# Kernel optimization log

Measured on AMD Instinct MI355X. Metric: run time of the kernel, lower is better.

## Reference

```python
import jax, jax.numpy as jnp
import numpy as np

N_SENS, N_HID, N_MOT = 10000, 400000, 1000
E_SH, E_HH, E_HM = 4_000_000, 16_000_000, 400_000
BETA, THR, SLOPE = 0.9, 1.0, 25.0  # snn.Leaky(beta, threshold), surrogate.fast_sigmoid(slope=25)

# Heaviside spike with fast-sigmoid surrogate gradient (matches snnTorch)
@jax.custom_vjp
def spike(x):
    return (x > 0).astype(x.dtype)

def _spike_fwd(x):
    return (x > 0).astype(x.dtype), x

def _spike_bwd(x, g):
    return (g / (SLOPE * jnp.abs(x) + 1.0) ** 2,)

spike.defvjp(_spike_fwd, _spike_bwd)

def lif(inp, mem):
    # snn.Leaky, reset_mechanism='zero': mem = beta*mem + I; spike; reset to 0 where spiked
    mem = BETA * mem + inp
    spk = spike(mem - THR)
    mem = mem - jax.lax.stop_gradient(spk) * mem  # reset detached, as in snnTorch
    return spk, mem

def spmm_t(pre_idx, post_idx, w, pre_spikes, n_post):
    # torch.sparse.mm(W^T, pre_spikes): gather pre activity along edges, scatter-add to post
    contrib = w * pre_spikes[pre_idx]          # [E]
    return jax.ops.segment_sum(contrib, post_idx, num_segments=n_post)

def setup_inputs() -> dict:
    key = jax.random.key(0)
    ks = jax.random.split(key, 16)
    std_sh = 1.0 / np.sqrt(N_SENS * 0.001)
    std_hh = 1.0 / np.sqrt(N_HID * 0.0001)
    std_hm = 1.0 / np.sqrt(N_HID * 0.001)
    return {
        "sensory_input": jax.random.uniform(ks[0], (N_SENS,), jnp.float32),
        "sensory_mem": jax.random.uniform(ks[1], (N_SENS,), jnp.float32),
        "hidden_mem": jax.random.uniform(ks[2], (N_HID,), jnp.float32),
        "motor_mem": jax.random.uniform(ks[3], (N_MOT,), jnp.float32),
        "hidden_prev_spikes": (jax.random.uniform(ks[4], (N_HID,)) < 0.05).astype(jnp.float32),
        "w_sh": jax.random.normal(ks[5], (E_SH,), jnp.float32) * std_sh,
        "w_hh": jax.random.normal(ks[6], (E_HH,), jnp.float32) * std_hh,
        "w_hm": jax.random.normal(ks[7], (E_HM,), jnp.float32) * std_hm,
        "sh_pre": jax.random.randint(ks[8], (E_SH,), 0, N_SENS, jnp.int32),
        "sh_post": jax.random.randint(ks[9], (E_SH,), 0, N_HID, jnp.int32),
        "hh_pre": jax.random.randint(ks[10], (E_HH,), 0, N_HID, jnp.int32),
        "hh_post": jax.random.randint(ks[11], (E_HH,), 0, N_HID, jnp.int32),
        "hm_pre": jax.random.randint(ks[12], (E_HM,), 0, N_HID, jnp.int32),
        "hm_post": jax.random.randint(ks[13], (E_HM,), 0, N_MOT, jnp.int32),
    }

def reference(sensory_input, sensory_mem, hidden_mem, motor_mem, hidden_prev_spikes,
              w_sh, w_hh, w_hm, sh_pre, sh_post, hh_pre, hh_post, hm_pre, hm_post):
    sens_spk, _ = lif(sensory_input * 5.0, sensory_mem)
    hid_in = spmm_t(sh_pre, sh_post, w_sh, sens_spk, N_HID)
    hid_in = hid_in + 0.5 * spmm_t(hh_pre, hh_post, w_hh, hidden_prev_spikes, N_HID)
    hid_spk, _ = lif(hid_in * 5.0, hidden_mem)
    mot_in = spmm_t(hm_pre, hm_post, w_hm, hid_spk, N_MOT)
    mot_spk, _ = lif(mot_in * 20.0, motor_mem)
    return mot_spk
```

## Files before the change

kernel.cpp:

```cpp
#include <hip/hip_runtime.h>


#define N_SENS 10000
#define N_HID  400000
#define N_MOT  1000

#define CHUNK_LOG 14
#define CHUNK     (1 << CHUNK_LOG)
#define NBUCKET   25
#define CAP       196608
#define NCOPY     20

#define SENS_MW   320
#define HID_MW    12512

#define BUF_SH    4096
#define BUF_HH    2048
#define EPT_SH    4
#define EPT_HH    8

#define NB_HM     128

__global__ void make_masks(const float* __restrict__ sens_in,
                           const float* __restrict__ sens_mem,
                           const float* __restrict__ hid_prev,
                           uint2* __restrict__ smask,
                           uint2* __restrict__ hmask,
                           float* __restrict__ extra,
                           int* __restrict__ cursors, int nb_sens) {
    bool pred = false;
    int i;
    uint2* dst;
    int maxw;
    if ((int)blockIdx.x < nb_sens) {
        if (blockIdx.x == 0 && threadIdx.x < 32) cursors[threadIdx.x] = 0;
        i = blockIdx.x * blockDim.x + threadIdx.x;
        if (i < N_SENS) pred = (0.9f * sens_mem[i] + 5.0f * sens_in[i]) > 1.0f;
        dst = smask; maxw = SENS_MW / 2;
    } else {
        i = (blockIdx.x - nb_sens) * blockDim.x + threadIdx.x;
        if (i < N_HID) { pred = (hid_prev[i] != 0.0f); extra[i] = 0.0f; }
        dst = hmask; maxw = HID_MW / 2;
    }
    unsigned long long b = __ballot(pred);
    if ((threadIdx.x & 63) == 0) {
        int w = i >> 6;
        if (w < maxw) dst[w] = make_uint2((unsigned)b, (unsigned)(b >> 32));
    }
}

template <int MW, int BUFCAP, int EPT>
__global__ __launch_bounds__(1024, 8)
void bin_gather(const int* __restrict__ pre, const int* __restrict__ post,
                const float* __restrict__ w, const unsigned* __restrict__ gmask,
                int n_e, float scale,
                uint2* __restrict__ pairs, int* __restrict__ gcursor,
                float* __restrict__ extra) {
    __shared__ unsigned sm[MW];
    __shared__ uint2 buf[BUFCAP];
    __shared__ int h[4][32];
    __shared__ int gb[32];
    __shared__ int lcur[32];
    __shared__ int total;

    const int tid = threadIdx.x;
    const int lane = tid & 63;
    for (int i = tid; i < MW / 4; i += 1024)
        ((uint4*)sm)[i] = ((const uint4*)gmask)[i];
    if (tid < 128) ((int*)h)[tid] = 0;
    if (tid == 0) total = 0;
    __syncthreads();

    const int base = blockIdx.x * (1024 * EPT) + tid;

    int pr[EPT];
    #pragma unroll
    for (int j = 0; j < EPT; ++j) {
        int e = base + j * 1024;
        pr[j] = (e < n_e) ? pre[e] : -1;
    }
    bool act[EPT];
    #pragma unroll
    for (int j = 0; j < EPT; ++j)
        act[j] = (pr[j] >= 0) && ((sm[pr[j] >> 5] >> (pr[j] & 31)) & 1u);
    unsigned p[EPT]; float wv[EPT];
    #pragma unroll
    for (int j = 0; j < EPT; ++j) {
        p[j] = 0; wv[j] = 0.0f;
        if (act[j]) {
            int e = base + j * 1024;
            p[j] = (unsigned)post[e];
            wv[j] = scale * w[e];
        }
    }
    #pragma unroll
    for (int j = 0; j < EPT; ++j) {
        unsigned long long m = __ballot(act[j]);
        if (!m) continue;
        int rank = __popcll(m & ((1ull << lane) - 1ull));
        int bse = 0;
        if (lane == 0) bse = atomicAdd(&total, __popcll(m));
        bse = __shfl(bse, 0);
        if (act[j]) {
            int k = bse + rank;
            if (k < BUFCAP) buf[k] = make_uint2(p[j], __float_as_uint(wv[j]));
            else atomicAdd(&extra[p[j]], wv[j]);
        }
    }
    __syncthreads();
    int tot = total; if (tot > BUFCAP) tot = BUFCAP;

    int rep = (tid >> 6) & 3;
    for (int k = tid; k < tot; k += 1024)
        atomicAdd(&h[rep][buf[k].x >> CHUNK_LOG], 1);
    __syncthreads();
    if (tid < NBUCKET) {
        int hb = h[0][tid] + h[1][tid] + h[2][tid] + h[3][tid];
        gb[tid] = hb ? atomicAdd(&gcursor[tid], hb) : 0;
        lcur[tid] = 0;
    }
    __syncthreads();

    for (int k = tid; k < tot; k += 1024) {
        uint2 u = buf[k];
        int b = u.x >> CHUNK_LOG;
        int s = atomicAdd(&lcur[b], 1);
        int pos = gb[b] + s;
        if (pos < CAP)
            pairs[(size_t)b * CAP + pos] =
                make_uint2(u.x & (CHUNK - 1), u.y);
        else
            atomicAdd(&extra[u.x], __uint_as_float(u.y));
    }
}

__global__ __launch_bounds__(1024, 8)
void accum_bucket(const uint2* __restrict__ pairs,
                  const int* __restrict__ cursors,
                  float* __restrict__ partials) {
    int bucket = blockIdx.x / NCOPY;
    int copy   = blockIdx.x % NCOPY;
    __shared__ float acc[CHUNK];
    for (int i = threadIdx.x; i < CHUNK; i += blockDim.x) acc[i] = 0.0f;
    __syncthreads();

    int count = cursors[bucket];
    if (count > CAP) count = CAP;
    int begin = (int)((long long)count * copy / NCOPY);
    int end   = (int)((long long)count * (copy + 1) / NCOPY);
    const uint2* src = pairs + (size_t)bucket * CAP;
    for (int i = begin + threadIdx.x; i < end; i += blockDim.x) {
        uint2 u = src[i];
        atomicAdd(&acc[u.x], __uint_as_float(u.y));
    }
    __syncthreads();
    float* dst = partials + ((size_t)bucket * NCOPY + copy) * CHUNK;
    for (int i = threadIdx.x; i < CHUNK; i += blockDim.x) dst[i] = acc[i];
}

__global__ void reduce_lif_hidden_mask(const float* __restrict__ partials,
                                       const float* __restrict__ extra,
                                       const float* __restrict__ mem,
                                       uint2* __restrict__ mask) {
    int i = blockIdx.x * blockDim.x + threadIdx.x;
    bool pred = false;
    if (i < N_HID) {
        int b = i >> CHUNK_LOG, local = i & (CHUNK - 1);
        const float* p = partials + (size_t)b * NCOPY * CHUNK + local;
        float sum = extra[i];
        #pragma unroll
        for (int c = 0; c < NCOPY; ++c) sum += p[(size_t)c * CHUNK];
        pred = (0.9f * mem[i] + 5.0f * sum) > 1.0f;
    }
    unsigned long long bal = __ballot(pred);
    if ((threadIdx.x & 63) == 0) {
        int w = i >> 6;
        if (w < HID_MW / 2)
            mask[w] = make_uint2((unsigned)bal, (unsigned)(bal >> 32));
    }
}

__global__ __launch_bounds__(512, 8)
void scatter_motor_mask(const int* __restrict__ pre,
                        const int* __restrict__ post,
                        const float* __restrict__ w,
                        const unsigned* __restrict__ gmask,
                        float* __restrict__ partials, int n_edges) {
    __shared__ float acc[N_MOT];
    for (int j = threadIdx.x; j < N_MOT; j += blockDim.x) acc[j] = 0.0f;
    __syncthreads();
    for (int e = blockIdx.x * blockDim.x + threadIdx.x; e < n_edges;
         e += gridDim.x * blockDim.x) {
        int pr = pre[e];
        if ((gmask[pr >> 5] >> (pr & 31)) & 1u)
            atomicAdd(&acc[post[e]], w[e]);
    }
    __syncthreads();
    float* out = partials + (size_t)blockIdx.x * N_MOT;
    for (int j = threadIdx.x; j < N_MOT; j += blockDim.x) out[j] = acc[j];
}

__global__ void reduce_lif_motor(const float* __restrict__ partials, int nb,
                                 const float* __restrict__ mem,
                                 float* __restrict__ out) {
    int m = blockIdx.x * blockDim.x + threadIdx.x;
    if (m >= N_MOT) return;
    float sum = 0.0f;
    for (int b = 0; b < nb; ++b) sum += partials[(size_t)b * N_MOT + m];
    float v = 0.9f * mem[m] + 20.0f * sum;
    out[m] = (v > 1.0f) ? 1.0f : 0.0f;
}

__global__ void lif_kernel(const float* __restrict__ inp,
                           const float* __restrict__ mem_in,
                           float* __restrict__ spk,
                           float scale, int n) {
    int i = blockIdx.x * blockDim.x + threadIdx.x;
    if (i < n) {
        float m = 0.9f * mem_in[i] + scale * inp[i];
        spk[i] = (m > 1.0f) ? 1.0f : 0.0f;
    }
}

__global__ void scatter_dev(const int* __restrict__ pre,
                            const int* __restrict__ post,
                            const float* __restrict__ w,
                            const float* __restrict__ spikes,
                            float* __restrict__ out,
                            float scale, int n_edges) {
    int e = blockIdx.x * blockDim.x + threadIdx.x;
    if (e >= n_edges) return;
    float s = spikes[pre[e]];
    if (s != 0.0f) atomicAdd(&out[post[e]], scale * w[e] * s);
}

__global__ void lif_hidden_direct(const float* __restrict__ hid_in,
                                  const float* __restrict__ mem,
                                  float* __restrict__ spk) {
    int i = blockIdx.x * blockDim.x + threadIdx.x;
    if (i >= N_HID) return;
    float m = 0.9f * mem[i] + 5.0f * hid_in[i];
    spk[i] = (m > 1.0f) ? 1.0f : 0.0f;
}

__global__ void scatter_motor_f(const int* __restrict__ pre,
                                const int* __restrict__ post,
                                const float* __restrict__ w,
                                const float* __restrict__ spikes,
                                float* __restrict__ partials, int n_edges) {
    __shared__ float acc[N_MOT];
    for (int j = threadIdx.x; j < N_MOT; j += blockDim.x) acc[j] = 0.0f;
    __syncthreads();
    for (int e = blockIdx.x * blockDim.x + threadIdx.x; e < n_edges;
         e += gridDim.x * blockDim.x) {
        float s = spikes[pre[e]];
        if (s != 0.0f) atomicAdd(&acc[post[e]], w[e] * s);
    }
    __syncthreads();
    float* out = partials + (size_t)blockIdx.x * N_MOT;
    for (int j = threadIdx.x; j < N_MOT; j += blockDim.x) out[j] = acc[j];
}

extern "C" void kernel_launch(void* const* d_in, const int* in_sizes, int n_in,
                              void* d_out, int out_size, void* d_ws, size_t ws_size,
                              hipStream_t stream) {
    const float* sensory_input = (const float*)d_in[0];
    const float* sensory_mem   = (const float*)d_in[1];
    const float* hidden_mem    = (const float*)d_in[2];
    const float* motor_mem     = (const float*)d_in[3];
    const float* hidden_prev   = (const float*)d_in[4];
    const float* w_sh          = (const float*)d_in[5];
    const float* w_hh          = (const float*)d_in[6];
    const float* w_hm          = (const float*)d_in[7];
    const int*   sh_pre        = (const int*)d_in[8];
    const int*   sh_post       = (const int*)d_in[9];
    const int*   hh_pre        = (const int*)d_in[10];
    const int*   hh_post       = (const int*)d_in[11];
    const int*   hm_pre        = (const int*)d_in[12];
    const int*   hm_post       = (const int*)d_in[13];
    const int e_sh = in_sizes[5];
    const int e_hh = in_sizes[6];
    const int e_hm = in_sizes[7];
    const int B = 256;

    size_t o_cursor = 0;
    size_t o_extra  = 32;
    size_t o_pairs  = o_extra + N_HID;
    size_t o_part   = o_pairs + (size_t)NBUCKET * CAP * 2;
    size_t o_smask  = o_part + (size_t)NBUCKET * NCOPY * CHUNK;
    size_t o_hmaskp = o_smask + SENS_MW;
    size_t o_hmasks = o_hmaskp + HID_MW;
    size_t o_mpart  = o_hmasks + HID_MW;
    size_t f_need   = o_mpart + (size_t)NB_HM * N_MOT;
    bool fast = (ws_size / sizeof(float)) >= f_need;

    float* ws = (float*)d_ws;
    if (fast) {
        int*      cursors = (int*)(ws + o_cursor);
        float*    extra   = ws + o_extra;
        uint2*    pairs   = (uint2*)(ws + o_pairs);
        float*    part    = ws + o_part;
        unsigned* smask   = (unsigned*)(ws + o_smask);
        unsigned* hmaskp  = (unsigned*)(ws + o_hmaskp);
        unsigned* hmasks  = (unsigned*)(ws + o_hmasks);
        float*    mpart   = ws + o_mpart;

        int nb_sens = (N_SENS + B - 1) / B;
        int nb_hidm = (N_HID + B - 1) / B;
        make_masks<<<nb_sens + nb_hidm, B, 0, stream>>>(
            sensory_input, sensory_mem, hidden_prev,
            (uint2*)smask, (uint2*)hmaskp, extra, cursors, nb_sens);

        int nb_sh = (e_sh + 1024 * EPT_SH - 1) / (1024 * EPT_SH);
        int nb_hh = (e_hh + 1024 * EPT_HH - 1) / (1024 * EPT_HH);
        bin_gather<SENS_MW, BUF_SH, EPT_SH><<<nb_sh, 1024, 0, stream>>>(
            sh_pre, sh_post, w_sh, smask, e_sh, 1.0f, pairs, cursors, extra);
        bin_gather<HID_MW, BUF_HH, EPT_HH><<<nb_hh, 1024, 0, stream>>>(
            hh_pre, hh_post, w_hh, hmaskp, e_hh, 0.5f, pairs, cursors, extra);

        accum_bucket<<<NBUCKET * NCOPY, 1024, 0, stream>>>(pairs, cursors, part);
        reduce_lif_hidden_mask<<<(N_HID + B - 1) / B, B, 0, stream>>>(
            part, extra, hidden_mem, (uint2*)hmasks);
        scatter_motor_mask<<<NB_HM, 512, 0, stream>>>(
            hm_pre, hm_post, w_hm, hmasks, mpart, e_hm);
        reduce_lif_motor<<<(N_MOT + B - 1) / B, B, 0, stream>>>(
            mpart, NB_HM, motor_mem, (float*)d_out);
    } else {
        float* hid_in   = ws;
        float* sens_spk = hid_in + N_HID;
        float* hid_spk  = sens_spk + 10016;
        float* mpart    = hid_spk + N_HID;
        hipMemsetAsync(hid_in, 0, (size_t)N_HID * sizeof(float), stream);
        lif_kernel<<<(N_SENS + B - 1) / B, B, 0, stream>>>(
            sensory_input, sensory_mem, sens_spk, 5.0f, N_SENS);
        scatter_dev<<<(e_sh + B - 1) / B, B, 0, stream>>>(
            sh_pre, sh_post, w_sh, sens_spk, hid_in, 1.0f, e_sh);
        scatter_dev<<<(e_hh + B - 1) / B, B, 0, stream>>>(
            hh_pre, hh_post, w_hh, hidden_prev, hid_in, 0.5f, e_hh);
        lif_hidden_direct<<<(N_HID + B - 1) / B, B, 0, stream>>>(
            hid_in, hidden_mem, hid_spk);
        scatter_motor_f<<<NB_HM, B, 0, stream>>>(
            hm_pre, hm_post, w_hm, hid_spk, mpart, e_hm);
        reduce_lif_motor<<<(N_MOT + B - 1) / B, B, 0, stream>>>(
            mpart, NB_HM, motor_mem, (float*)d_out);
    }
}
```

Baseline: 356.4 us.

## Compact active edges per thread with wave scan, retune tiles, cache motor mask in LDS

The binning kernel now builds a per-thread bitmask of active edges and uses one wave-wide prefix scan plus one shared atomic per wave to reserve buffer slots. This replaces a ballot and atomic per unrolled slot and loads post and weight only for active edges. Edges per thread rise (8 for sensory, 32 for recurrent), the sensory buffer doubles, and accumulation copies and motor blocks are halved. The motor scatter now stages the hidden spike mask in shared memory and runs 1024-thread blocks. Fewer, larger blocks may reduce parallelism and latency hiding, and higher per-block counts raise the chance of overflow into global atomics.

```diff
diff --git a/kernel.cpp b/kernel.cpp
--- a/kernel.cpp
+++ b/kernel.cpp
@@ -9,17 +9,17 @@
 #define CHUNK     (1 << CHUNK_LOG)
 #define NBUCKET   25
 #define CAP       196608
-#define NCOPY     20
+#define NCOPY     10
 
 #define SENS_MW   320
 #define HID_MW    12512
 
-#define BUF_SH    4096
+#define EPT_SH    8
+#define BUF_SH    8192
+#define EPT_HH    32
 #define BUF_HH    2048
-#define EPT_SH    4
-#define EPT_HH    8
-
-#define NB_HM     128
+
+#define NB_HM     64
 
 __global__ void make_masks(const float* __restrict__ sens_in,
                            const float* __restrict__ sens_mem,
@@ -51,11 +51,11 @@
 
 template <int MW, int BUFCAP, int EPT>
 __global__ __launch_bounds__(1024, 8)
-void bin_gather(const int* __restrict__ pre, const int* __restrict__ post,
-                const float* __restrict__ w, const unsigned* __restrict__ gmask,
-                int n_e, float scale,
-                uint2* __restrict__ pairs, int* __restrict__ gcursor,
-                float* __restrict__ extra) {
+void bin_scan(const int* __restrict__ pre, const int* __restrict__ post,
+              const float* __restrict__ w, const unsigned* __restrict__ gmask,
+              int n_e, float scale,
+              uint2* __restrict__ pairs, int* __restrict__ gcursor,
+              float* __restrict__ extra) {
     __shared__ unsigned sm[MW];
     __shared__ uint2 buf[BUFCAP];
     __shared__ int h[4][32];
@@ -73,38 +73,38 @@
 
     const int base = blockIdx.x * (1024 * EPT) + tid;
 
-    int pr[EPT];
+    unsigned am = 0;
     #pragma unroll
     for (int j = 0; j < EPT; ++j) {
         int e = base + j * 1024;
-        pr[j] = (e < n_e) ? pre[e] : -1;
-    }
-    bool act[EPT];
+        if (e < n_e) {
+            int pr = pre[e];
+            if ((sm[pr >> 5] >> (pr & 31)) & 1u) am |= (1u << j);
+        }
+    }
+    int cnt = __popc(am);
+
+    int inc = cnt;
     #pragma unroll
-    for (int j = 0; j < EPT; ++j)
-        act[j] = (pr[j] >= 0) && ((sm[pr[j] >> 5] >> (pr[j] & 31)) & 1u);
-    unsigned p[EPT]; float wv[EPT];
+    for (int d = 1; d < 64; d <<= 1) {
+        int n = __shfl_up(inc, d);
+        if (lane >= d) inc += n;
+    }
+    int wtot = __shfl(inc, 63);
+    int wbase = 0;
+    if (lane == 63 && wtot) wbase = atomicAdd(&total, wtot);
+    wbase = __shfl(wbase, 63);
+    int off = wbase + inc - cnt;
+
     #pragma unroll
     for (int j = 0; j < EPT; ++j) {
-        p[j] = 0; wv[j] = 0.0f;
-        if (act[j]) {
+        if ((am >> j) & 1u) {
             int e = base + j * 1024;
-            p[j] = (unsigned)post[e];
-            wv[j] = scale * w[e];
-        }
-    }
-    #pragma unroll
-    for (int j = 0; j < EPT; ++j) {
-        unsigned long long m = __ballot(act[j]);
-        if (!m) continue;
-        int rank = __popcll(m & ((1ull << lane) - 1ull));
-        int bse = 0;
-        if (lane == 0) bse = atomicAdd(&total, __popcll(m));
-        bse = __shfl(bse, 0);
-        if (act[j]) {
-            int k = bse + rank;
-            if (k < BUFCAP) buf[k] = make_uint2(p[j], __float_as_uint(wv[j]));
-            else atomicAdd(&extra[p[j]], wv[j]);
+            unsigned p = (unsigned)post[e];
+            float wv = scale * w[e];
+            if (off < BUFCAP) buf[off] = make_uint2(p, __float_as_uint(wv));
+            else atomicAdd(&extra[p], wv);
+            ++off;
         }
     }
     __syncthreads();
@@ -180,19 +180,22 @@
     }
 }
 
-__global__ __launch_bounds__(512, 8)
+__global__ __launch_bounds__(1024, 8)
 void scatter_motor_mask(const int* __restrict__ pre,
                         const int* __restrict__ post,
                         const float* __restrict__ w,
                         const unsigned* __restrict__ gmask,
                         float* __restrict__ partials, int n_edges) {
     __shared__ float acc[N_MOT];
+    __shared__ unsigned sm[HID_MW];
+    for (int i = threadIdx.x; i < HID_MW / 4; i += blockDim.x)
+        ((uint4*)sm)[i] = ((const uint4*)gmask)[i];
     for (int j = threadIdx.x; j < N_MOT; j += blockDim.x) acc[j] = 0.0f;
     __syncthreads();
     for (int e = blockIdx.x * blockDim.x + threadIdx.x; e < n_edges;
          e += gridDim.x * blockDim.x) {
         int pr = pre[e];
-        if ((gmask[pr >> 5] >> (pr & 31)) & 1u)
+        if ((sm[pr >> 5] >> (pr & 31)) & 1u)
             atomicAdd(&acc[post[e]], w[e]);
     }
     __syncthreads();
@@ -313,15 +316,15 @@
 
         int nb_sh = (e_sh + 1024 * EPT_SH - 1) / (1024 * EPT_SH);
         int nb_hh = (e_hh + 1024 * EPT_HH - 1) / (1024 * EPT_HH);
-        bin_gather<SENS_MW, BUF_SH, EPT_SH><<<nb_sh, 1024, 0, stream>>>(
+        bin_scan<SENS_MW, BUF_SH, EPT_SH><<<nb_sh, 1024, 0, stream>>>(
             sh_pre, sh_post, w_sh, smask, e_sh, 1.0f, pairs, cursors, extra);
-        bin_gather<HID_MW, BUF_HH, EPT_HH><<<nb_hh, 1024, 0, stream>>>(
+        bin_scan<HID_MW, BUF_HH, EPT_HH><<<nb_hh, 1024, 0, stream>>>(
             hh_pre, hh_post, w_hh, hmaskp, e_hh, 0.5f, pairs, cursors, extra);
 
         accum_bucket<<<NBUCKET * NCOPY, 1024, 0, stream>>>(pairs, cursors, part);
         reduce_lif_hidden_mask<<<(N_HID + B - 1) / B, B, 0, stream>>>(
             part, extra, hidden_mem, (uint2*)hmasks);
-        scatter_motor_mask<<<NB_HM, 512, 0, stream>>>(
+        scatter_motor_mask<<<NB_HM, 1024, 0, stream>>>(
             hm_pre, hm_post, w_hm, hmasks, mpart, e_hm);
         reduce_lif_motor<<<(N_MOT + B - 1) / B, B, 0, stream>>>(
             mpart, NB_HM, motor_mem, (float*)d_out);
```

After: 338.2 us. 1.05x faster.
